# Kernel tuning notes

Measured on AMD Instinct MI355X. Metric: run time of the kernel, lower is better.

Reference implementation:

```python
import jax, jax.numpy as jnp
import numpy as np

EPS = 1e-5
SLOPE = 0.01  # LeakyReLU default negative_slope


def conv3(x, w):
    # x: [B,C,D,H,W], w: [O,I,3,3,3]; SubMConv3d on a dense grid == dense SAME conv, no bias
    return jax.lax.conv_general_dilated(
        x, w, window_strides=(1, 1, 1), padding='SAME',
        dimension_numbers=('NCDHW', 'OIDHW', 'NCDHW'))


def bn_c(x, g, b, m, v):
    # BatchNorm1d (eval) over channel axis 1 of [B,C,D,H,W]
    s = (1.0, -1, 1, 1, 1)
    return (x - m.reshape(1, -1, 1, 1, 1)) * (g.reshape(1, -1, 1, 1, 1) * jax.lax.rsqrt(v.reshape(1, -1, 1, 1, 1) + EPS)) + b.reshape(1, -1, 1, 1, 1)


def bn_f(x, g, b, m, v):
    # BatchNorm1d (eval) over last (feature) axis
    return (x - m) * (g * jax.lax.rsqrt(v + EPS)) + b


def lrelu(x):
    return jnp.where(x > 0, x, SLOPE * x)


def setup_inputs() -> dict:
    key = jax.random.key(0)
    ks = jax.random.split(key, 32)
    B, C, D, H, W = 2, 256, 64, 64, 16
    N = 100000
    init_size, emb = 32, 3

    fea = jax.random.normal(ks[0], (B, C, D, H, W), dtype=jnp.float32)
    gi0 = jax.random.randint(ks[1], (B, N), 0, D)
    gi1 = jax.random.randint(ks[2], (B, N), 0, H)
    gi2 = jax.random.randint(ks[3], (B, N), 0, W)
    grid_ind = jnp.stack([gi0, gi1, gi2], axis=-1).astype(jnp.int32)  # [B,N,3]
    xyz = jax.random.normal(ks[4], (B, N, 3), dtype=jnp.float32)

    def bn_params(k, c):
        k1, k2, k3, k4 = jax.random.split(k, 4)
        return (1.0 + 0.1 * jax.random.normal(k1, (c,), jnp.float32),
                0.1 * jax.random.normal(k2, (c,), jnp.float32),
                0.1 * jax.random.normal(k3, (c,), jnp.float32),
                0.5 + jax.random.uniform(k4, (c,), jnp.float32))

    W1 = jax.random.normal(ks[5], (C, C, 3, 3, 3), jnp.float32) * (1.0 / np.sqrt(27 * C))
    g1, b1, m1, v1 = bn_params(ks[6], C)
    W2 = jax.random.normal(ks[7], (2 * init_size, C, 3, 3, 3), jnp.float32) * (1.0 / np.sqrt(27 * C))
    g2, b2, m2, v2 = bn_params(ks[8], 2 * init_size)
    W3 = jax.random.normal(ks[9], (init_size, 2 * init_size, 3, 3, 3), jnp.float32) * (1.0 / np.sqrt(27 * 2 * init_size))
    g3, b3, m3, v3 = bn_params(ks[10], init_size)

    Wo1 = jax.random.normal(ks[11], (init_size + 3, init_size), jnp.float32) * (1.0 / np.sqrt(init_size + 3))
    bo1 = 0.01 * jax.random.normal(ks[12], (init_size,), jnp.float32)
    go, bo, mo, vo = bn_params(ks[13], init_size)
    Wo2 = jax.random.normal(ks[14], (init_size, emb), jnp.float32) * (1.0 / np.sqrt(init_size))
    bo2 = 0.01 * jax.random.normal(ks[15], (emb,), jnp.float32)

    return dict(fea=fea, grid_ind=grid_ind, xyz=xyz,
                W1=W1, g1=g1, b1=b1, m1=m1, v1=v1,
                W2=W2, g2=g2, b2=b2, m2=m2, v2=v2,
                W3=W3, g3=g3, b3=b3, m3=m3, v3=v3,
                Wo1=Wo1, bo1=bo1, go=go, bo=bo, mo=mo, vo=vo,
                Wo2=Wo2, bo2=bo2)


def reference(fea, grid_ind, xyz,
              W1, g1, b1, m1, v1,
              W2, g2, b2, m2, v2,
              W3, g3, b3, m3, v3,
              Wo1, bo1, go, bo, mo, vo,
              Wo2, bo2):
    # sparse conv stack (dense-grid equivalent)
    x = lrelu(bn_c(conv3(fea, W1), g1, b1, m1, v1))
    x = lrelu(bn_c(conv3(x, W2), g2, b2, m2, v2))
    x = lrelu(bn_c(conv3(x, W3), g3, b3, m3, v3))  # [B, init_size, D, H, W]

    # fea.dense().permute(0,2,3,4,1) -> [B, D, H, W, C]; per-point gather
    xg = jnp.transpose(x, (0, 2, 3, 4, 1))
    B = xg.shape[0]
    bidx = jnp.arange(B)[:, None]  # [B,1]
    pt = xg[bidx, grid_ind[:, :, 0], grid_ind[:, :, 1], grid_ind[:, :, 2]]  # [B, N, init_size]

    # concat xyz, Linear -> BN -> ReLU -> Linear
    h = jnp.concatenate([pt, xyz[:, :, :3]], axis=-1)
    h = jax.nn.relu(bn_f(h @ Wo1 + bo1, go, bo, mo, vo))
    return h @ Wo2 + bo2  # [B, N, embedding_dim]
```

## Files before the change

### kernel.cpp

```cpp
#include <hip/hip_runtime.h>
#include <stdint.h>

#define EPS 1e-5f
#define SLOPE 0.01f

typedef short bf16x8 __attribute__((ext_vector_type(8)));
typedef float f32x4 __attribute__((ext_vector_type(4)));

__device__ __forceinline__ uint16_t f2bf(float x) {
  union { float f; uint32_t u; } v; v.f = x;
  return (uint16_t)((v.u + 0x7fffu + ((v.u >> 16) & 1u)) >> 16);
}

__device__ __forceinline__ void g2lds16(const void* g, void* l) {
  __builtin_amdgcn_global_load_lds(
      (const __attribute__((address_space(1))) void*)g,
      (__attribute__((address_space(3))) void*)l, 16, 0, 0);
}

__global__ void prep_bn(const float* g1, const float* b1, const float* m1, const float* v1,
                        const float* g2, const float* b2, const float* m2, const float* v2,
                        const float* g3, const float* b3, const float* m3, const float* v3,
                        const float* go, const float* bo, const float* mo, const float* vo,
                        const float* bo1,
                        float* s1, float* be1, float* s2, float* be2,
                        float* s3, float* be3, float* so, float* beo) {
  int t = threadIdx.x;
  if (t < 256) { float s = g1[t] / sqrtf(v1[t] + EPS); s1[t] = s; be1[t] = b1[t] - m1[t] * s; }
  if (t < 64)  { float s = g2[t] / sqrtf(v2[t] + EPS); s2[t] = s; be2[t] = b2[t] - m2[t] * s; }
  if (t < 32)  { float s = g3[t] / sqrtf(v3[t] + EPS); s3[t] = s; be3[t] = b3[t] - m3[t] * s; }
  if (t < 32)  { float s = go[t] / sqrtf(vo[t] + EPS); so[t] = s; beo[t] = bo[t] + (bo1[t] - mo[t]) * s; }
}

__global__ void wtrans(const float* __restrict__ W, uint16_t* __restrict__ Wt,
                       int CO, int CI) {
  int idx = blockIdx.x * 256 + threadIdx.x;
  int total = CO * CI * 27;
  if (idx >= total) return;
  int t = idx / (CO * CI);
  int rem = idx % (CO * CI);
  int co = rem / CI, ci = rem % CI;
  Wt[idx] = f2bf(W[((size_t)co * CI + ci) * 27 + t]);
}

__global__ __launch_bounds__(256) void transpose_fea(const float* __restrict__ fea,
                                                     uint16_t* __restrict__ pad0) {
  int tid = threadIdx.x;
  int idx = blockIdx.x;
  int half = idx & 1;
  int q = (idx >> 1) & 3;
  int d = (idx >> 3) & 63;
  int b = idx >> 9;
  int s = q * 256 + tid;
  int h = s >> 4, w = s & 15;
  const float* src = fea + (size_t)(b * 256 + half * 128) * 65536 + (size_t)d * 1024 + s;
  uint16_t* dst = pad0 + ((size_t)b * 78408 +
                          (size_t)((d + 1) * 1188 + (h + 1) * 18 + (w + 1))) * 256 + half * 128;
#pragma unroll 4
  for (int c8 = 0; c8 < 16; ++c8) {
    uint16_t v[8];
#pragma unroll
    for (int j = 0; j < 8; ++j)
      v[j] = f2bf(src[(size_t)(c8 * 8 + j) * 65536]);
    *(uint4*)&dst[c8 * 8] = *(uint4*)v;
  }
}

template <int CI, int CO, int NTILE, int WM, int WN, bool LAST>
__global__ __launch_bounds__(256) void conv_mfma(const uint16_t* __restrict__ padIn,
                                                 const uint16_t* __restrict__ Wt,
                                                 const float* __restrict__ bnS,
                                                 const float* __restrict__ bnB,
                                                 uint16_t* __restrict__ padOut,
                                                 float* __restrict__ x3out) {
  constexpr int MPW = 128 / WM;
  constexpr int NPW = NTILE / WN;
  constexpr int MSUB = MPW / 16;
  constexpr int NSUB = NPW / 16;
  constexpr int BPASS = NTILE / 32;
  constexpr int KC = CI / 64;

  __shared__ __align__(16) uint16_t Alds[20 * 8 * 64];
  __shared__ __align__(16) uint16_t Blds[NTILE * 64];

  const int tid = threadIdx.x;
  const int lane = tid & 63;
  const int wv = tid >> 6;
  const int wvm = wv / WN;
  const int wvn = wv % WN;

  const int mt = blockIdx.x;
  const int b = mt >> 9;
  const int r = mt & 511;
  const int d = r >> 3;
  const int h0 = (r & 7) << 3;
  const int n0 = blockIdx.y * NTILE;

  const int subswB = (tid & 7) ^ ((tid >> 3) & 7);
  const int rowB0 = tid >> 3;
  const int mhA = lane >> 3;
  const int unA = lane & 7;

  f32x4 acc[MSUB][NSUB] = {};

  const size_t bOffIn = (size_t)b * 78408 * CI;

  for (int dh = 0; dh < 9; ++dh) {
    const int kd = dh / 3, kh = dh % 3;
    const size_t Abase = bOffIn + (size_t)((d + kd) * 1188 + (h0 + kh) * 18) * CI;
    for (int kc = 0; kc < KC; ++kc) {
      for (int kw = 0; kw < 3; ++kw) {
        __syncthreads();
        if (kw == 0) {
          const uint16_t* ag = padIn + Abase + kc * 64 + (size_t)mhA * (18 * CI);
#pragma unroll
          for (int p = 0; p < 5; ++p) {
            int wp = wv * 5 + p;
            int gu = unA ^ (wp & 7);
            g2lds16(ag + (size_t)wp * CI + gu * 8, (char*)Alds + wp * 1024);
          }
        }
        {
          const uint16_t* bg = Wt + (size_t)((dh * 3 + kw) * CO + n0) * CI + kc * 64 + subswB * 8;
#pragma unroll
          for (int p = 0; p < BPASS; ++p)
            g2lds16(bg + (size_t)(rowB0 + 32 * p) * CI, (char*)Blds + p * 4096 + wv * 1024);
        }
        __syncthreads();
#pragma unroll
        for (int ks = 0; ks < 2; ++ks) {
          bf16x8 af[MSUB], bfr[NSUB];
#pragma unroll
          for (int mi = 0; mi < MSUB; ++mi) {
            int wq = (lane & 15) + kw;
            int u = (ks * 4 + (lane >> 4)) ^ (wq & 7);
            af[mi] = *(const bf16x8*)&Alds[wq * 512 + (wvm * MSUB + mi) * 64 + u * 8];
          }
#pragma unroll
          for (int ni = 0; ni < NSUB; ++ni) {
            int row = wvn * NPW + ni * 16 + (lane & 15);
            int u = (ks * 4 + (lane >> 4)) ^ (row & 7);
            bfr[ni] = *(const bf16x8*)&Blds[row * 64 + u * 8];
          }
#pragma unroll
          for (int mi = 0; mi < MSUB; ++mi)
#pragma unroll
            for (int ni = 0; ni < NSUB; ++ni)
              acc[mi][ni] = __builtin_amdgcn_mfma_f32_16x16x32_bf16(af[mi], bfr[ni], acc[mi][ni], 0, 0, 0);
        }
      }
    }
  }

  const int col = lane & 15;
  const int quad = lane >> 4;
#pragma unroll
  for (int ni = 0; ni < NSUB; ++ni) {
    const int co = n0 + wvn * NPW + ni * 16 + col;
    const float sv = bnS[co];
    const float bv = bnB[co];
#pragma unroll
    for (int mi = 0; mi < MSUB; ++mi) {
#pragma unroll
      for (int rr = 0; rr < 4; ++rr) {
        int m = wvm * MPW + mi * 16 + quad * 4 + rr;
        float v = acc[mi][ni][rr] * sv + bv;
        v = v > 0.f ? v : SLOPE * v;
        int mh = m >> 4, w = m & 15;
        if (!LAST) {
          size_t o = ((size_t)b * 78408 +
                      (size_t)((d + 1) * 1188 + (h0 + mh + 1) * 18 + (w + 1))) * CO + co;
          padOut[o] = f2bf(v);
        } else {
          size_t o = ((size_t)b * 65536 + (size_t)((d * 64 + h0 + mh) * 16 + w)) * 32 + co;
          x3out[o] = v;
        }
      }
    }
  }
}

__global__ __launch_bounds__(256) void gather_mlp(const float* __restrict__ x3,
                                                  const int* __restrict__ gidx,
                                                  const float* __restrict__ xyz,
                                                  const float* __restrict__ Wo1,
                                                  const float* __restrict__ so,
                                                  const float* __restrict__ beo,
                                                  const float* __restrict__ Wo2,
                                                  const float* __restrict__ bo2,
                                                  float* __restrict__ out) {
  __shared__ __align__(16) float w1[35 * 32];
  __shared__ float w2[32 * 3];
  __shared__ float sS[32], sB[32], b2s[3];
  int tid = threadIdx.x;
  for (int i = tid; i < 1120; i += 256) w1[i] = Wo1[i];
  if (tid < 96) w2[tid] = Wo2[tid];
  if (tid < 32) { sS[tid] = so[tid]; sB[tid] = beo[tid]; }
  if (tid < 3) b2s[tid] = bo2[tid];
  __syncthreads();

  int idx = blockIdx.x * 256 + tid;
  if (idx >= 200000) return;
  int b = idx >= 100000 ? 1 : 0;
  int gb = idx * 3;
  int i0 = gidx[gb], i1 = gidx[gb + 1], i2 = gidx[gb + 2];
  const float* pt = x3 + ((size_t)b * 65536 + (size_t)((i0 * 64 + i1) * 16 + i2)) * 32;

  float h[35];
#pragma unroll
  for (int q = 0; q < 8; ++q) {
    float4 v = *(const float4*)(pt + q * 4);
    h[q * 4] = v.x; h[q * 4 + 1] = v.y; h[q * 4 + 2] = v.z; h[q * 4 + 3] = v.w;
  }
  h[32] = xyz[gb]; h[33] = xyz[gb + 1]; h[34] = xyz[gb + 2];

  float a[32];
#pragma unroll
  for (int j = 0; j < 32; ++j) a[j] = 0.f;
#pragma unroll
  for (int k = 0; k < 35; ++k) {
    float hk = h[k];
    const float4* wr = (const float4*)(w1 + k * 32);
#pragma unroll
    for (int q = 0; q < 8; ++q) {
      float4 wv = wr[q];
      a[q * 4 + 0] += hk * wv.x;
      a[q * 4 + 1] += hk * wv.y;
      a[q * 4 + 2] += hk * wv.z;
      a[q * 4 + 3] += hk * wv.w;
    }
  }
  float o0 = b2s[0], o1 = b2s[1], o2 = b2s[2];
#pragma unroll
  for (int j = 0; j < 32; ++j) {
    float y = a[j] * sS[j] + sB[j];
    y = y > 0.f ? y : 0.f;
    o0 += y * w2[j * 3 + 0];
    o1 += y * w2[j * 3 + 1];
    o2 += y * w2[j * 3 + 2];
  }
  out[gb] = o0; out[gb + 1] = o1; out[gb + 2] = o2;
}

extern "C" void kernel_launch(void* const* d_in, const int* in_sizes, int n_in,
                              void* d_out, int out_size, void* d_ws, size_t ws_size,
                              hipStream_t stream) {
  (void)in_sizes; (void)n_in; (void)out_size;
  if (ws_size < 165130000) return;

  const float* fea = (const float*)d_in[0];
  const int*   gidx = (const int*)d_in[1];
  const float* xyz = (const float*)d_in[2];
  const float* W1 = (const float*)d_in[3];
  const float* g1 = (const float*)d_in[4];
  const float* b1 = (const float*)d_in[5];
  const float* m1 = (const float*)d_in[6];
  const float* v1 = (const float*)d_in[7];
  const float* W2 = (const float*)d_in[8];
  const float* g2 = (const float*)d_in[9];
  const float* b2 = (const float*)d_in[10];
  const float* m2 = (const float*)d_in[11];
  const float* v2 = (const float*)d_in[12];
  const float* W3 = (const float*)d_in[13];
  const float* g3 = (const float*)d_in[14];
  const float* b3 = (const float*)d_in[15];
  const float* m3 = (const float*)d_in[16];
  const float* v3 = (const float*)d_in[17];
  const float* Wo1 = (const float*)d_in[18];
  const float* bo1 = (const float*)d_in[19];
  const float* go = (const float*)d_in[20];
  const float* bo = (const float*)d_in[21];
  const float* mo = (const float*)d_in[22];
  const float* vo = (const float*)d_in[23];
  const float* Wo2 = (const float*)d_in[24];
  const float* bo2 = (const float*)d_in[25];

  char* ws = (char*)d_ws;
  uint16_t* pad0 = (uint16_t*)(ws);
  uint16_t* pad1 = (uint16_t*)(ws + 80289792);
  uint16_t* Wt1 = (uint16_t*)(ws + 160579584);
  uint16_t* Wt2 = (uint16_t*)(ws + 164118528);
  uint16_t* Wt3 = (uint16_t*)(ws + 165003264);
  float* s1  = (float*)(ws + 165113856 + 0 * 1024);
  float* be1 = (float*)(ws + 165113856 + 1 * 1024);
  float* s2  = (float*)(ws + 165113856 + 2 * 1024);
  float* be2 = (float*)(ws + 165113856 + 3 * 1024);
  float* s3  = (float*)(ws + 165113856 + 4 * 1024);
  float* be3 = (float*)(ws + 165113856 + 5 * 1024);
  float* so  = (float*)(ws + 165113856 + 6 * 1024);
  float* beo = (float*)(ws + 165113856 + 7 * 1024);
  uint16_t* pad2 = (uint16_t*)(ws);
  float* x3 = (float*)(ws + 20072448);

  hipMemsetAsync(ws, 0, 160579584, stream);

  prep_bn<<<1, 256, 0, stream>>>(g1, b1, m1, v1, g2, b2, m2, v2, g3, b3, m3, v3,
                                 go, bo, mo, vo, bo1, s1, be1, s2, be2, s3, be3, so, beo);
  wtrans<<<6912, 256, 0, stream>>>(W1, Wt1, 256, 256);
  wtrans<<<1728, 256, 0, stream>>>(W2, Wt2, 64, 256);
  wtrans<<<216, 256, 0, stream>>>(W3, Wt3, 32, 64);
  transpose_fea<<<1024, 256, 0, stream>>>(fea, pad0);

  conv_mfma<256, 256, 128, 2, 2, false>
      <<<dim3(1024, 2), 256, 0, stream>>>(pad0, Wt1, s1, be1, pad1, nullptr);

  hipMemsetAsync(pad2, 0, 20072448, stream);

  conv_mfma<256, 64, 64, 2, 2, false>
      <<<dim3(1024, 1), 256, 0, stream>>>(pad1, Wt2, s2, be2, pad2, nullptr);

  conv_mfma<64, 32, 32, 4, 1, true>
      <<<dim3(1024, 1), 256, 0, stream>>>(pad2, Wt3, s3, be3, nullptr, x3);

  gather_mlp<<<782, 256, 0, stream>>>(x3, gidx, xyz, Wo1, so, beo, Wo2, bo2, (float*)d_out);
}
```

Before: 1.046 ms.

## Use full-output-channel tiles and taller M tiles in conv kernels

Each conv block now covers all output channels (NTILE = CO), so the grid no longer splits over N. This avoids reloading the same input A tile per N slice. Conv2 and conv3 use 16-row M tiles (256 voxels per block), loading A in two halves, with half as many blocks. Launch bounds request 2 blocks per CU. In exchange, conv1 carries a much larger per-wave accumulator set, which raises register pressure and risks spills or lower occupancy.

```diff
diff --git a/kernel.cpp b/kernel.cpp
--- a/kernel.cpp
+++ b/kernel.cpp
@@ -66,21 +66,26 @@
   }
 }
 
-template <int CI, int CO, int NTILE, int WM, int WN, bool LAST>
-__global__ __launch_bounds__(256) void conv_mfma(const uint16_t* __restrict__ padIn,
-                                                 const uint16_t* __restrict__ Wt,
-                                                 const float* __restrict__ bnS,
-                                                 const float* __restrict__ bnB,
-                                                 uint16_t* __restrict__ padOut,
-                                                 float* __restrict__ x3out) {
-  constexpr int MPW = 128 / WM;
+template <int CI, int CO, int MH, int WM, int WN, bool LAST>
+__global__ __launch_bounds__(256, 2) void conv_mfma(const uint16_t* __restrict__ padIn,
+                                                    const uint16_t* __restrict__ Wt,
+                                                    const float* __restrict__ bnS,
+                                                    const float* __restrict__ bnB,
+                                                    uint16_t* __restrict__ padOut,
+                                                    float* __restrict__ x3out) {
+  constexpr int NTILE = CO;
+  constexpr int MTILE = MH * 16;
+  constexpr int MPW = MTILE / WM;
   constexpr int NPW = NTILE / WN;
   constexpr int MSUB = MPW / 16;
   constexpr int NSUB = NPW / 16;
   constexpr int BPASS = NTILE / 32;
   constexpr int KC = CI / 64;
-
-  __shared__ __align__(16) uint16_t Alds[20 * 8 * 64];
+  constexpr int HB = 64 / MH;
+  constexpr int HALF = MH / 8;
+  constexpr int ROWSTR = 18 * CI;
+
+  __shared__ __align__(16) uint16_t Alds[20 * MH * 64];
   __shared__ __align__(16) uint16_t Blds[NTILE * 64];
 
   const int tid = threadIdx.x;
@@ -90,16 +95,13 @@
   const int wvn = wv % WN;
 
   const int mt = blockIdx.x;
-  const int b = mt >> 9;
-  const int r = mt & 511;
-  const int d = r >> 3;
-  const int h0 = (r & 7) << 3;
-  const int n0 = blockIdx.y * NTILE;
+  const int b = mt / (64 * HB);
+  const int r = mt % (64 * HB);
+  const int d = r / HB;
+  const int h0 = (r % HB) * MH;
 
   const int subswB = (tid & 7) ^ ((tid >> 3) & 7);
   const int rowB0 = tid >> 3;
-  const int mhA = lane >> 3;
-  const int unA = lane & 7;
 
   f32x4 acc[MSUB][NSUB] = {};
 
@@ -112,16 +114,19 @@
       for (int kw = 0; kw < 3; ++kw) {
         __syncthreads();
         if (kw == 0) {
-          const uint16_t* ag = padIn + Abase + kc * 64 + (size_t)mhA * (18 * CI);
+          const uint16_t* agBase = padIn + Abase + kc * 64 + (size_t)(lane >> 3) * ROWSTR;
 #pragma unroll
           for (int p = 0; p < 5; ++p) {
             int wp = wv * 5 + p;
-            int gu = unA ^ (wp & 7);
-            g2lds16(ag + (size_t)wp * CI + gu * 8, (char*)Alds + wp * 1024);
+            int gu = (lane & 7) ^ (wp & 7);
+#pragma unroll
+            for (int hf = 0; hf < HALF; ++hf)
+              g2lds16(agBase + (size_t)(hf * 8) * ROWSTR + wp * CI + gu * 8,
+                      (char*)Alds + wp * (MH * 128) + hf * 1024);
           }
         }
         {
-          const uint16_t* bg = Wt + (size_t)((dh * 3 + kw) * CO + n0) * CI + kc * 64 + subswB * 8;
+          const uint16_t* bg = Wt + (size_t)((dh * 3 + kw) * CO) * CI + kc * 64 + subswB * 8;
 #pragma unroll
           for (int p = 0; p < BPASS; ++p)
             g2lds16(bg + (size_t)(rowB0 + 32 * p) * CI, (char*)Blds + p * 4096 + wv * 1024);
@@ -134,7 +139,8 @@
           for (int mi = 0; mi < MSUB; ++mi) {
             int wq = (lane & 15) + kw;
             int u = (ks * 4 + (lane >> 4)) ^ (wq & 7);
-            af[mi] = *(const bf16x8*)&Alds[wq * 512 + (wvm * MSUB + mi) * 64 + u * 8];
+            int mhIdx = wvm * MSUB + mi;
+            af[mi] = *(const bf16x8*)&Alds[wq * (MH * 64) + mhIdx * 64 + u * 8];
           }
 #pragma unroll
           for (int ni = 0; ni < NSUB; ++ni) {
@@ -156,7 +162,7 @@
   const int quad = lane >> 4;
 #pragma unroll
   for (int ni = 0; ni < NSUB; ++ni) {
-    const int co = n0 + wvn * NPW + ni * 16 + col;
+    const int co = wvn * NPW + ni * 16 + col;
     const float sv = bnS[co];
     const float bv = bnB[co];
 #pragma unroll
@@ -301,16 +307,16 @@
   wtrans<<<216, 256, 0, stream>>>(W3, Wt3, 32, 64);
   transpose_fea<<<1024, 256, 0, stream>>>(fea, pad0);
 
-  conv_mfma<256, 256, 128, 2, 2, false>
-      <<<dim3(1024, 2), 256, 0, stream>>>(pad0, Wt1, s1, be1, pad1, nullptr);
+  conv_mfma<256, 256, 8, 2, 2, false>
+      <<<1024, 256, 0, stream>>>(pad0, Wt1, s1, be1, pad1, nullptr);
 
   hipMemsetAsync(pad2, 0, 20072448, stream);
 
-  conv_mfma<256, 64, 64, 2, 2, false>
-      <<<dim3(1024, 1), 256, 0, stream>>>(pad1, Wt2, s2, be2, pad2, nullptr);
-
-  conv_mfma<64, 32, 32, 4, 1, true>
-      <<<dim3(1024, 1), 256, 0, stream>>>(pad2, Wt3, s3, be3, nullptr, x3);
+  conv_mfma<256, 64, 16, 4, 1, false>
+      <<<512, 256, 0, stream>>>(pad1, Wt2, s2, be2, pad2, nullptr);
+
+  conv_mfma<64, 32, 16, 4, 1, true>
+      <<<512, 256, 0, stream>>>(pad2, Wt3, s3, be3, nullptr, x3);
 
   gather_mlp<<<782, 256, 0, stream>>>(x3, gidx, xyz, Wo1, so, beo, Wo2, bo2, (float*)d_out);
 }
```

Result: no change. 1.042 ms (-0.3%).
